# Kernel optimization log

Hardware: AMD Instinct MI355X
Metric: run time of the kernel (lower is better)

The kernel has to match this reference:

```python
import jax, jax.numpy as jnp
import numpy as np


def setup_inputs() -> dict:
    key = jax.random.key(0)
    k1, k2, k3 = jax.random.split(key, 3)
    B, C, T = 8, 16, 131072
    O, n_keep, n_discard = 16, 48, 16
    x = jax.random.normal(k1, (B, C, T), dtype=jnp.float32)
    weight = jax.random.normal(k2, (O, C * n_keep), dtype=jnp.float32) * 0.05
    bias = jax.random.normal(k3, (O,), dtype=jnp.float32) * 0.05
    return {"x": x, "weight": weight, "bias": bias,
            "n_discard": n_discard, "n_keep": n_keep}


def reference(x, weight, bias, n_discard, n_keep):
    # x: (B, C, T); weight: (O, C*n_keep); bias: (O,)
    B, C, T = x.shape
    O = weight.shape[0]
    S = n_keep + n_discard              # window (group) size
    G = -(-T // S)                      # number of groups
    pad = G * S - T
    xp = jnp.pad(x, ((0, 0), (0, 0), (0, pad)))
    # per-timestep weight blocks: (n_keep, C, O), zero-padded for discarded frames -> (S, C, O)
    w = weight.reshape(O, C, n_keep).transpose(2, 1, 0)
    w = jnp.pad(w, ((n_discard, 0), (0, 0), (0, 0)))
    # group the time axis: (B, C, G, S)
    xg = xp.reshape(B, C, G, S)
    # per-timestep projection then causal cumsum within each window
    y = jnp.einsum('bcgs,sco->bgso', xg, w)   # (B, G, S, O)
    y = jnp.cumsum(y, axis=2) + bias          # reset every window; bias seeds each window
    y = y.transpose(0, 3, 1, 2).reshape(B, O, G * S)
    return y[..., :T]
```

## Files before the change

kernel.cpp:

```cpp
#include <hip/hip_runtime.h>


#define CC 16
#define TT 131072
#define OO 16
#define NK 48
#define ND 16
#define WPB 4
#define GG 2048

#define SCAN_STEP(CTRL, RMASK)                                                  \
  {                                                                             \
    int t_ = __builtin_amdgcn_update_dpp(0, __float_as_int(v), (CTRL), (RMASK), \
                                         0xf, true);                            \
    v += __int_as_float(t_);                                                    \
  }

__device__ __forceinline__ float wave_scan64(float v) {
  SCAN_STEP(0x111, 0xf)
  SCAN_STEP(0x112, 0xf)
  SCAN_STEP(0x114, 0xf)
  SCAN_STEP(0x118, 0xf)
  SCAN_STEP(0x142, 0xa)
  SCAN_STEP(0x143, 0xc)
  return v;
}

__global__ __launch_bounds__(256, 4) void cfl_kernel(
    const float* __restrict__ x, const float* __restrict__ weight,
    const float* __restrict__ bias, float* __restrict__ out) {
  __shared__ float tile[4 * 256 * 4];

  const int tid = threadIdx.x;
  const int lane = tid & 63;
  const int wid = tid >> 6;

  const int n0 = blockIdx.x * WPB;
  const int b = n0 >> 11;
  const int t0 = (n0 & (GG - 1)) * 64;

  const float* xb = x + (size_t)b * CC * TT + t0;
#pragma unroll
  for (int c = 0; c < CC; ++c) {
    float v = xb[(size_t)c * TT + tid];
    tile[(((c >> 2) * 256 + tid) << 2) + (c & 3)] = v;
  }
  __syncthreads();

  float* ob = out + (size_t)b * OO * TT + t0;

#pragma unroll
  for (int p = 0; p < 2; ++p) {
    const int o0 = p * 4 + wid;

    float w0[CC], w1[CC];
#pragma unroll
    for (int c = 0; c < CC; ++c) {
      w0[c] = (lane >= ND) ? weight[o0 * (CC * NK) + c * NK + (lane - ND)] : 0.f;
      w1[c] = (lane >= ND) ? weight[(o0 + 8) * (CC * NK) + c * NK + (lane - ND)] : 0.f;
    }
    const float b0 = bias[o0];
    const float b1 = bias[o0 + 8];

#pragma unroll
    for (int k = 0; k < WPB; ++k) {
      const int t = k * 64 + lane;
      float4 xq0 = *(const float4*)&tile[(0 * 256 + t) << 2];
      float4 xq1 = *(const float4*)&tile[(1 * 256 + t) << 2];
      float4 xq2 = *(const float4*)&tile[(2 * 256 + t) << 2];
      float4 xq3 = *(const float4*)&tile[(3 * 256 + t) << 2];

      float p0 = 0.f, p1 = 0.f;
      p0 = fmaf(xq0.x, w0[0], p0);  p1 = fmaf(xq0.x, w1[0], p1);
      p0 = fmaf(xq0.y, w0[1], p0);  p1 = fmaf(xq0.y, w1[1], p1);
      p0 = fmaf(xq0.z, w0[2], p0);  p1 = fmaf(xq0.z, w1[2], p1);
      p0 = fmaf(xq0.w, w0[3], p0);  p1 = fmaf(xq0.w, w1[3], p1);
      p0 = fmaf(xq1.x, w0[4], p0);  p1 = fmaf(xq1.x, w1[4], p1);
      p0 = fmaf(xq1.y, w0[5], p0);  p1 = fmaf(xq1.y, w1[5], p1);
      p0 = fmaf(xq1.z, w0[6], p0);  p1 = fmaf(xq1.z, w1[6], p1);
      p0 = fmaf(xq1.w, w0[7], p0);  p1 = fmaf(xq1.w, w1[7], p1);
      p0 = fmaf(xq2.x, w0[8], p0);  p1 = fmaf(xq2.x, w1[8], p1);
      p0 = fmaf(xq2.y, w0[9], p0);  p1 = fmaf(xq2.y, w1[9], p1);
      p0 = fmaf(xq2.z, w0[10], p0); p1 = fmaf(xq2.z, w1[10], p1);
      p0 = fmaf(xq2.w, w0[11], p0); p1 = fmaf(xq2.w, w1[11], p1);
      p0 = fmaf(xq3.x, w0[12], p0); p1 = fmaf(xq3.x, w1[12], p1);
      p0 = fmaf(xq3.y, w0[13], p0); p1 = fmaf(xq3.y, w1[13], p1);
      p0 = fmaf(xq3.z, w0[14], p0); p1 = fmaf(xq3.z, w1[14], p1);
      p0 = fmaf(xq3.w, w0[15], p0); p1 = fmaf(xq3.w, w1[15], p1);

      const float cs0 = wave_scan64(p0);
      const float cs1 = wave_scan64(p1);
      ob[(size_t)o0 * TT + t] = cs0 + b0;
      ob[(size_t)(o0 + 8) * TT + t] = cs1 + b1;
    }
  }
}

extern "C" void kernel_launch(void* const* d_in, const int* in_sizes, int n_in,
                              void* d_out, int out_size, void* d_ws, size_t ws_size,
                              hipStream_t stream) {
  const float* x = (const float*)d_in[0];
  const float* weight = (const float*)d_in[1];
  const float* bias = (const float*)d_in[2];
  float* out = (float*)d_out;

  cfl_kernel<<<4096, 256, 0, stream>>>(x, weight, bias, out);
}
```

Before: 31.23 us.

## Make blocks persistent over 8 time tiles with register-prefetched input and per-wave weights

Each block now has 512 threads (8 waves, one output pair per wave) and loops over 8 consecutive 256-step time tiles instead of handling one tile. Weights are loaded into registers once per block rather than once per output pass. The next tile's input is prefetched into registers while the current tile is computed, then written to shared memory between two barriers. The grid shrinks from 4096 to 512 blocks, which cuts per-block setup and weight reloads but lowers block count and adds two barriers per tile.

```diff
diff --git a/kernel.cpp b/kernel.cpp
--- a/kernel.cpp
+++ b/kernel.cpp
@@ -6,8 +6,10 @@
 #define OO 16
 #define NK 48
 #define ND 16
-#define WPB 4
 #define GG 2048
+#define NT 8
+#define WPT 4
+#define WPB (NT * WPT)
 
 #define SCAN_STEP(CTRL, RMASK)                                                  \
   {                                                                             \
@@ -26,7 +28,7 @@
   return v;
 }
 
-__global__ __launch_bounds__(256, 4) void cfl_kernel(
+__global__ __launch_bounds__(512, 4) void cfl_kernel(
     const float* __restrict__ x, const float* __restrict__ weight,
     const float* __restrict__ bias, float* __restrict__ out) {
   __shared__ float tile[4 * 256 * 4];
@@ -37,38 +39,54 @@
 
   const int n0 = blockIdx.x * WPB;
   const int b = n0 >> 11;
-  const int t0 = (n0 & (GG - 1)) * 64;
+  const int t00 = (n0 & (GG - 1)) * 64;
 
-  const float* xb = x + (size_t)b * CC * TT + t0;
+  const int o0 = wid, o1 = wid + 8;
+  float w0[CC], w1[CC];
 #pragma unroll
   for (int c = 0; c < CC; ++c) {
-    float v = xb[(size_t)c * TT + tid];
-    tile[(((c >> 2) * 256 + tid) << 2) + (c & 3)] = v;
+    float a = 0.f, bq = 0.f;
+    if (lane >= ND) {
+      a = weight[o0 * (CC * NK) + c * NK + (lane - ND)];
+      bq = weight[o1 * (CC * NK) + c * NK + (lane - ND)];
+    }
+    asm volatile("" : "+v"(a), "+v"(bq));
+    w0[c] = a;
+    w1[c] = bq;
+  }
+  const float b0 = bias[o0];
+  const float b1 = bias[o1];
+
+  const int st = tid & 255;
+  const int ch = (tid >> 8) * 8;
+  const float* xb = x + (size_t)b * CC * TT + t00 + st;
+  float* ob = out + (size_t)b * OO * TT + t00;
+
+  float xs[8];
+#pragma unroll
+  for (int i = 0; i < 8; ++i) xs[i] = xb[(size_t)(ch + i) * TT];
+#pragma unroll
+  for (int i = 0; i < 8; ++i) {
+    const int c = ch + i;
+    tile[(((c >> 2) * 256 + st) << 2) + (c & 3)] = xs[i];
   }
   __syncthreads();
 
-  float* ob = out + (size_t)b * OO * TT + t0;
+  for (int tt = 0; tt < NT; ++tt) {
+    if (tt + 1 < NT) {
+#pragma unroll
+      for (int i = 0; i < 8; ++i)
+        xs[i] = xb[(size_t)(ch + i) * TT + (tt + 1) * 256];
+    }
 
+    const int tb = tt * 256;
 #pragma unroll
-  for (int p = 0; p < 2; ++p) {
-    const int o0 = p * 4 + wid;
-
-    float w0[CC], w1[CC];
-#pragma unroll
-    for (int c = 0; c < CC; ++c) {
-      w0[c] = (lane >= ND) ? weight[o0 * (CC * NK) + c * NK + (lane - ND)] : 0.f;
-      w1[c] = (lane >= ND) ? weight[(o0 + 8) * (CC * NK) + c * NK + (lane - ND)] : 0.f;
-    }
-    const float b0 = bias[o0];
-    const float b1 = bias[o0 + 8];
-
-#pragma unroll
-    for (int k = 0; k < WPB; ++k) {
+    for (int k = 0; k < WPT; ++k) {
       const int t = k * 64 + lane;
-      float4 xq0 = *(const float4*)&tile[(0 * 256 + t) << 2];
-      float4 xq1 = *(const float4*)&tile[(1 * 256 + t) << 2];
-      float4 xq2 = *(const float4*)&tile[(2 * 256 + t) << 2];
-      float4 xq3 = *(const float4*)&tile[(3 * 256 + t) << 2];
+      const float4 xq0 = *(const float4*)&tile[(0 * 256 + t) << 2];
+      const float4 xq1 = *(const float4*)&tile[(1 * 256 + t) << 2];
+      const float4 xq2 = *(const float4*)&tile[(2 * 256 + t) << 2];
+      const float4 xq3 = *(const float4*)&tile[(3 * 256 + t) << 2];
 
       float p0 = 0.f, p1 = 0.f;
       p0 = fmaf(xq0.x, w0[0], p0);  p1 = fmaf(xq0.x, w1[0], p1);
@@ -90,8 +108,18 @@
 
       const float cs0 = wave_scan64(p0);
       const float cs1 = wave_scan64(p1);
-      ob[(size_t)o0 * TT + t] = cs0 + b0;
-      ob[(size_t)(o0 + 8) * TT + t] = cs1 + b1;
+      ob[(size_t)o0 * TT + tb + t] = cs0 + b0;
+      ob[(size_t)o1 * TT + tb + t] = cs1 + b1;
+    }
+
+    if (tt + 1 < NT) {
+      __syncthreads();
+#pragma unroll
+      for (int i = 0; i < 8; ++i) {
+        const int c = ch + i;
+        tile[(((c >> 2) * 256 + st) << 2) + (c & 3)] = xs[i];
+      }
+      __syncthreads();
     }
   }
 }
@@ -104,5 +132,5 @@
   const float* bias = (const float*)d_in[2];
   float* out = (float*)d_out;
 
-  cfl_kernel<<<4096, 256, 0, stream>>>(x, weight, bias, out);
+  cfl_kernel<<<512, 512, 0, stream>>>(x, weight, bias, out);
 }
```

Result: slower. 32.61 us (+4.4%).
